# Optimization experiments

Measured on AMD Instinct MI355X. Metric: run time of the kernel, lower is better.

The kernel has to match this reference:

```python
import jax, jax.numpy as jnp
import numpy as np

E = 768          # embed_dim
H = 12           # n_attention_heads
D = E // H       # head_embed_dim = 64
S = 197          # seq_len (196 patches + CLS)
MRD = 13         # max_relative_dist
GRID = 14        # sqrt(S - 1)
B = 64
NUM_EMB = 2 * MRD + 1 + 1  # embedding table rows (index 0 reserved for CLS)


def _relative_distances(pos):
    # pos: (S-1,) int. distances clamped, shifted to [1, 2*MRD+1], padded with 0 for CLS.
    d = pos[None, :] - pos[:, None]
    d = np.clip(d, -MRD, MRD) + MRD + 1
    d = np.pad(d, ((1, 0), (1, 0)), constant_values=0)
    return jnp.asarray(d, dtype=jnp.int32)  # (S, S)


def setup_inputs() -> dict:
    key = jax.random.key(0)
    ks = jax.random.split(key, 16)
    s_lin = 1.0 / np.sqrt(E)
    inp = {
        "x": jax.random.normal(ks[0], (B, S, E), jnp.float32),
        "Wq": jax.random.normal(ks[1], (E, E), jnp.float32) * s_lin,
        "bq": jnp.zeros((E,), jnp.float32),
        "Wk": jax.random.normal(ks[2], (E, E), jnp.float32) * s_lin,
        "bk": jnp.zeros((E,), jnp.float32),
        "Wv": jax.random.normal(ks[3], (E, E), jnp.float32) * s_lin,
        "bv": jnp.zeros((E,), jnp.float32),
        "Wo": jax.random.normal(ks[4], (E, E), jnp.float32) * s_lin,
        "bo": jnp.zeros((E,), jnp.float32),
        "q_tab_x": jax.random.normal(ks[5], (NUM_EMB, D // 2), jnp.float32),
        "q_tab_y": jax.random.normal(ks[6], (NUM_EMB, D // 2), jnp.float32),
        "v_tab_x": jax.random.normal(ks[7], (NUM_EMB, D // 2), jnp.float32),
        "v_tab_y": jax.random.normal(ks[8], (NUM_EMB, D // 2), jnp.float32),
    }
    p = np.arange(S - 1)
    inp["x_dist"] = _relative_distances(p % GRID)   # (S, S) int32
    inp["y_dist"] = _relative_distances(p // GRID)  # (S, S) int32
    return inp


def reference(x, Wq, bq, Wk, bk, Wv, bv, Wo, bo,
              q_tab_x, q_tab_y, v_tab_x, v_tab_y, x_dist, y_dist):
    b, s, e = x.shape
    # QKV projections -> (b, h, s, d)
    xq = (x @ Wq.T + bq).reshape(b, s, H, D).transpose(0, 2, 1, 3)
    xk = (x @ Wk.T + bk).reshape(b, s, H, D).transpose(0, 2, 1, 3)
    xv = (x @ Wv.T + bv).reshape(b, s, H, D).transpose(0, 2, 1, 3)

    # content logits
    attn = jnp.einsum('bhqd,bhkd->bhqk', xq, xk)

    # query relative-position logits: pos embedding (q, k, d) gathered from x/y tables
    q_pos = jnp.concatenate([q_tab_x[x_dist], q_tab_y[y_dist]], axis=-1)  # (s, s, d)
    attn = attn + jnp.einsum('bhqd,qkd->bhqk', xq, q_pos)

    attn = jax.nn.softmax(attn / np.float32(np.sqrt(D)), axis=-1)

    out = jnp.einsum('bhqk,bhkd->bhqd', attn, xv)

    # value relative-position contribution
    v_pos = jnp.concatenate([v_tab_x[x_dist], v_tab_y[y_dist]], axis=-1)  # (s, s, d)
    out = out + jnp.einsum('bhqk,qkd->bhqd', attn, v_pos)

    out = out.transpose(0, 2, 1, 3).reshape(b, s, e)
    return out @ Wo.T + bo
```

## Files before the change

kernel.cpp:

```cpp
#include <hip/hip_runtime.h>
#include <math.h>

#define SEQ 197
#define EMB 768
#define NH  12
#define HD  64
#define NE  28
#define SK  208
#define VP  232
#define PP  232
#define EP  232
#define HP  68
#define TP  66
#define NW  7
#define NT  448

typedef __attribute__((ext_vector_type(8))) __bf16 bf16x8;
typedef __attribute__((ext_vector_type(4))) float  f32x4;

__device__ __forceinline__ unsigned short f2bf(float f) {
    unsigned u = __float_as_uint(f);
    u += 0x7fffu + ((u >> 16) & 1u);
    return (unsigned short)(u >> 16);
}
__device__ __forceinline__ float bfl(unsigned u) { return __uint_as_float(u << 16); }

__device__ __forceinline__ void gl_lds16(const ushort* g, ushort* l) {
    __builtin_amdgcn_global_load_lds(
        (const __attribute__((address_space(1))) unsigned int*)g,
        (__attribute__((address_space(3))) unsigned int*)l, 16, 0, 0);
}

__global__ void cvt_k(const float* __restrict__ src, ushort* __restrict__ dst, int n4) {
    int i = blockIdx.x * 256 + threadIdx.x;
    if (i < n4) {
        float4 v = ((const float4*)src)[i];
        ushort4 o = { f2bf(v.x), f2bf(v.y), f2bf(v.z), f2bf(v.w) };
        ((ushort4*)dst)[i] = o;
    }
}

__global__ void cvt_w4(const float* __restrict__ wq, const float* __restrict__ wk,
                       const float* __restrict__ wv, const float* __restrict__ wo,
                       ushort* __restrict__ wqkv, ushort* __restrict__ wob) {
    int i = blockIdx.x * 256 + threadIdx.x;
    if (i >= 4 * 147456) return;
    int seg = i / 147456, r = i - seg * 147456;
    const float* s = (seg == 0) ? wq : (seg == 1) ? wk : (seg == 2) ? wv : wo;
    float4 v = ((const float4*)s)[r];
    ushort4 o = { f2bf(v.x), f2bf(v.y), f2bf(v.z), f2bf(v.w) };
    if (seg < 3) ((ushort4*)wqkv)[(size_t)seg * 147456 + r] = o;
    else         ((ushort4*)wob)[r] = o;
}

__global__ __launch_bounds__(256) void rxy_gemm(
    const ushort* __restrict__ xq,
    const float* __restrict__ qtx, const float* __restrict__ qty,
    ushort* __restrict__ r_o)
{
    __shared__ __align__(16) ushort qtab_s[64][66];

    const int bh = blockIdx.x;
    const size_t base = (size_t)bh * SEQ * HD;
    const int tid = threadIdx.x;
    const int w = tid >> 6, lane = tid & 63;
    const int g = lane >> 4, c15 = lane & 15;

    for (int idx = tid; idx < 64 * 64; idx += 256) {
        const int e = idx >> 6, d = idx & 63;
        float v = 0.f;
        if (e < 28)      { if (d < 32)  v = qtx[e * 32 + d]; }
        else if (e < 56) { if (d >= 32) v = qty[(e - 28) * 32 + (d - 32)]; }
        qtab_s[e][d] = f2bf(v);
    }
    __syncthreads();

    for (int qt = w; qt < 13; qt += 4) {
        const int qrow = qt * 16 + c15;
        const int qld = (qrow < SEQ) ? qrow : SEQ - 1;
        const bf16x8 qa0 = *(const bf16x8*)(xq + base + (size_t)qld * HD + g * 8);
        const bf16x8 qa1 = *(const bf16x8*)(xq + base + (size_t)qld * HD + 32 + g * 8);
#pragma unroll
        for (int et = 0; et < 4; et++) {
            bf16x8 t0 = *(const bf16x8*)&qtab_s[et * 16 + c15][g * 8];
            bf16x8 t1 = *(const bf16x8*)&qtab_s[et * 16 + c15][32 + g * 8];
            f32x4 a = (f32x4)0.f;
            a = __builtin_amdgcn_mfma_f32_16x16x32_bf16(qa0, t0, a, 0, 0, 0);
            a = __builtin_amdgcn_mfma_f32_16x16x32_bf16(qa1, t1, a, 0, 0, 0);
#pragma unroll
            for (int r = 0; r < 4; r++) {
                const int q = qt * 16 + g * 4 + r;
                const int e = et * 16 + c15;
                if (q < SEQ && e < 56)
                    r_o[((size_t)bh * SEQ + q) * 56 + e] = f2bf(a[r]);
            }
        }
    }
}

template<int MODE>
__global__ __launch_bounds__(256, 2) void gemm_k64(
    const ushort* __restrict__ A, const ushort* __restrict__ W,
    const float* __restrict__ b0, const float* __restrict__ b1, const float* __restrict__ b2,
    ushort* __restrict__ q_o, ushort* __restrict__ k_o, ushort* __restrict__ v_o,
    float* __restrict__ f_o, int M)
{
    __shared__ __align__(16) ushort As[128 * 64];
    __shared__ __align__(16) ushort Bs[128 * 64];

    const int tid  = threadIdx.x;
    const int w    = tid >> 6, lane = tid & 63;
    const int wr   = w >> 1,  wc   = w & 1;

    const int nmt = gridDim.x, nnt = gridDim.y;
    const int lin = blockIdx.y * nmt + blockIdx.x;
    const int gsz = 8 * nnt;
    const int grp = lin / gsz;
    const int rr  = lin - grp * gsz;
    int mig = nmt - grp * 8; if (mig > 8) mig = 8;
    const int mt  = grp * 8 + rr % mig;
    const int nt  = rr / mig;
    const int m0  = mt * 128;
    const int n0  = nt * 128;

    int arow[4], asrc[4];
#pragma unroll
    for (int i = 0; i < 4; i++) {
        const int gidx = tid + i * 256;
        const int row = gidx >> 3, ch = gidx & 7;
        arow[i] = row;
        asrc[i] = (ch ^ (row & 7)) * 8;
    }

    f32x4 acc[4][4];
#pragma unroll
    for (int m = 0; m < 4; m++)
#pragma unroll
        for (int n = 0; n < 4; n++) acc[m][n] = (f32x4)0.f;

    for (int k0 = 0; k0 < EMB; k0 += 64) {
#pragma unroll
        for (int i = 0; i < 4; i++) {
            int ra = m0 + arow[i]; if (ra >= M) ra = M - 1;
            gl_lds16(A + (size_t)ra * EMB + k0 + asrc[i], As + (tid + i * 256) * 8);
            gl_lds16(W + (size_t)(n0 + arow[i]) * EMB + k0 + asrc[i], Bs + (tid + i * 256) * 8);
        }
        __syncthreads();

#pragma unroll
        for (int kk = 0; kk < 2; kk++) {
            bf16x8 af[4], bfr[4];
#pragma unroll
            for (int m = 0; m < 4; m++) {
                const int row = wr * 64 + m * 16 + (lane & 15);
                af[m] = *(const bf16x8*)&As[row * 64 + (((kk * 4 + (lane >> 4)) ^ (row & 7)) << 3)];
            }
#pragma unroll
            for (int n = 0; n < 4; n++) {
                const int row = wc * 64 + n * 16 + (lane & 15);
                bfr[n] = *(const bf16x8*)&Bs[row * 64 + (((kk * 4 + (lane >> 4)) ^ (row & 7)) << 3)];
            }
#pragma unroll
            for (int m = 0; m < 4; m++)
#pragma unroll
                for (int n = 0; n < 4; n++)
                    acc[m][n] = __builtin_amdgcn_mfma_f32_16x16x32_bf16(af[m], bfr[n], acc[m][n], 0, 0, 0);
        }
        __syncthreads();
    }

    const int mat = n0 / EMB;
    const int nr  = n0 - mat * EMB;
    const float* bias = (mat == 0) ? b0 : (mat == 1) ? b1 : b2;
    ushort* dst = (mat == 0) ? q_o : (mat == 1) ? k_o : v_o;

#pragma unroll
    for (int m = 0; m < 4; m++) {
#pragma unroll
        for (int r = 0; r < 4; r++) {
            const int gm = m0 + wr * 64 + m * 16 + (lane >> 4) * 4 + r;
            if (gm >= M) continue;
            const int bb = gm / SEQ, ss = gm - bb * SEQ;
#pragma unroll
            for (int n = 0; n < 4; n++) {
                const int col = nr + wc * 64 + n * 16 + (lane & 15);
                if (MODE == 0) {
                    const float v = acc[m][n][r] + bias[col];
                    dst[(((size_t)bb * NH + (col >> 6)) * SEQ + ss) * HD + (col & 63)] = f2bf(v);
                } else {
                    f_o[(size_t)gm * EMB + col] = acc[m][n][r] + b0[col];
                }
            }
        }
    }
}

__global__ __launch_bounds__(NT) void attn_mfma(
    const ushort* __restrict__ xq, const ushort* __restrict__ xk, const ushort* __restrict__ xv,
    const ushort* __restrict__ rxy_g,
    const float* __restrict__ v_tab_x, const float* __restrict__ v_tab_y,
    const int* __restrict__ x_dist, const int* __restrict__ y_dist,
    ushort* __restrict__ ao)
{
    __shared__ __align__(16) ushort K_s[SK * HD];
    __shared__ __align__(16) ushort EXYs_s[SK * 40];
    __shared__ __align__(16) ushort EXYT_s[32 * EP];
    __shared__ __align__(16) ushort VT_s[HD * VP];
    __shared__ __align__(16) ushort P_s[NW * 16 * PP];
    __shared__ __align__(16) ushort vt_s[HD * TP];
    __shared__ __align__(16) ushort h_s[NW][16][HP];

    const int bh = blockIdx.x;
    const int b  = bh / NH;
    const int h  = bh % NH;
    const size_t base = (size_t)bh * SEQ * HD;
    const ushort* __restrict__ rxy_b = rxy_g + (size_t)bh * SEQ * 56;
    const int tid = threadIdx.x;
    const int w = tid >> 6, lane = tid & 63;
    const int g = lane >> 4, c15 = lane & 15;

    for (int idx = tid; idx < SK * 8; idx += NT) {
        const int r = idx >> 3, c = idx & 7;
        uint4 v = make_uint4(0, 0, 0, 0);
        if (r < SEQ) v = *(const uint4*)(xk + base + r * HD + c * 8);
        *(uint4*)&K_s[r * HD + ((c ^ (r & 7)) << 3)] = v;
    }
    for (int idx = tid; idx < SK * 40 / 8; idx += NT)
        *(uint4*)&EXYs_s[idx * 8] = make_uint4(0, 0, 0, 0);
    for (int idx = tid; idx < 32 * EP / 8; idx += NT)
        *(uint4*)&EXYT_s[idx * 8] = make_uint4(0, 0, 0, 0);
    for (int idx = tid; idx < HD * (VP - SEQ); idx += NT) {
        const int d = idx / (VP - SEQ), k = SEQ + idx - d * (VP - SEQ);
        VT_s[d * VP + k] = 0;
    }
    for (int idx = tid; idx < NW * 16 * PP / 8; idx += NT)
        *(uint4*)&P_s[idx * 8] = make_uint4(0, 0, 0, 0);
    for (int idx = tid; idx < 16 * 8 * 13; idx += NT) {
        const int kq = idx & 15, t = idx >> 4;
        const int db = t & 7, kh = t >> 3;
        const int k = kh * 16 + kq;
        if (k >= SEQ) continue;
        uint4 v = *(const uint4*)(xv + base + k * HD + db * 8);
        ushort* col = &VT_s[(db * 8) * VP + k];
        col[0 * VP] = (ushort)(v.x); col[1 * VP] = (ushort)(v.x >> 16);
        col[2 * VP] = (ushort)(v.y); col[3 * VP] = (ushort)(v.y >> 16);
        col[4 * VP] = (ushort)(v.z); col[5 * VP] = (ushort)(v.z >> 16);
        col[6 * VP] = (ushort)(v.w); col[7 * VP] = (ushort)(v.w >> 16);
    }
    for (int idx = tid; idx < HD * 64; idx += NT) {
        const int d = idx >> 6, e = idx & 63;
        float v = 0.f;
        if (d < 32) { if (e < 28) v = v_tab_x[e * 32 + d]; }
        else        { if (e >= 28 && e < 56) v = v_tab_y[(e - 28) * 32 + (d - 32)]; }
        vt_s[d * TP + e] = f2bf(v);
    }
    __syncthreads();
    for (int k = tid; k < SEQ; k += NT) {
        const int cx = (k == 0) ? 14 : (x_dist[SEQ + k] - 14);
        const int cy = (k == 0) ? 14 : (y_dist[SEQ + k] - 14);
        const ushort one = 0x3f80;
        EXYs_s[k * 40 + cx]        = one;
        EXYs_s[k * 40 + 16 + cy]   = one;
        EXYT_s[cx * EP + k]        = one;
        EXYT_s[(16 + cy) * EP + k] = one;
    }
    __syncthreads();

    for (int qt = w; qt < 13; qt += NW) {
        const int qrow = qt * 16 + c15;
        const int qld  = (qrow < SEQ) ? qrow : (SEQ - 1);
        const bf16x8 qa0 = *(const bf16x8*)(xq + base + (size_t)qld * HD + g * 8);
        const bf16x8 qa1 = *(const bf16x8*)(xq + base + (size_t)qld * HD + 32 + g * 8);

        uint4 up;
        {
            const ushort* rrow = rxy_b + qld * 56;
            const int cxq = (qld > 0) ? (x_dist[SEQ + qld] - 14) : 0;
            const int cyq = (qld > 0) ? (y_dist[SEQ + qld] - 14) : 0;
            unsigned uu[4] = {0, 0, 0, 0};
#pragma unroll
            for (int j = 0; j < 8; j++) {
                const int c = g * 8 + j;
                ushort v;
                if (qld == 0)      v = (c == 15 || c == 31) ? (ushort)0 : rrow[(c < 16) ? 0 : 28];
                else if (c < 14)   v = rrow[c - cxq + 14];
                else if (c == 14)  v = rrow[0];
                else if (c == 15)  v = 0;
                else if (c < 30)   v = rrow[28 + (c - 16) - cyq + 14];
                else if (c == 30)  v = rrow[28];
                else               v = 0;
                uu[j >> 1] |= ((unsigned)v) << ((j & 1) * 16);
            }
            up.x = uu[0]; up.y = uu[1]; up.z = uu[2]; up.w = uu[3];
        }
        const bf16x8 qa2 = *(bf16x8*)&up;

        {
            uint4* hz = (uint4*)h_s[w];
            for (int i = lane; i < 16 * HP / 8; i += 64) hz[i] = make_uint4(0, 0, 0, 0);
        }

        const int q4 = qt * 16 + 4 * g;
        float sum[4] = {0.f, 0.f, 0.f, 0.f};

#pragma unroll
        for (int kt = 0; kt < 13; kt++) {
            const int kr = kt * 16 + c15;
            bf16x8 kf0 = *(const bf16x8*)&K_s[kr * HD + (((0 + g) ^ (kr & 7)) << 3)];
            bf16x8 kf1 = *(const bf16x8*)&K_s[kr * HD + (((4 + g) ^ (kr & 7)) << 3)];
            bf16x8 kf2 = *(const bf16x8*)&EXYs_s[kr * 40 + g * 8];
            f32x4 a = (f32x4)0.f;
            a = __builtin_amdgcn_mfma_f32_16x16x32_bf16(qa0, kf0, a, 0, 0, 0);
            a = __builtin_amdgcn_mfma_f32_16x16x32_bf16(qa1, kf1, a, 0, 0, 0);
            a = __builtin_amdgcn_mfma_f32_16x16x32_bf16(qa2, kf2, a, 0, 0, 0);
#pragma unroll
            for (int r = 0; r < 4; r++) {
                const float l = a[r] * 0.125f - 8.0f;
                const float p = (kr < SEQ) ? __expf(l) : 0.f;
                sum[r] += p;
                P_s[(w * 16 + 4 * g + r) * PP + kr] = f2bf(p);
            }
        }
        float inv[4];
#pragma unroll
        for (int r = 0; r < 4; r++) {
            sum[r] += __shfl_xor(sum[r], 1);
            sum[r] += __shfl_xor(sum[r], 2);
            sum[r] += __shfl_xor(sum[r], 4);
            sum[r] += __shfl_xor(sum[r], 8);
            inv[r] = 1.f / sum[r];
        }

        f32x4 px0 = (f32x4)0.f, px1 = (f32x4)0.f;
#pragma unroll
        for (int ks = 0; ks < 7; ks++) {
            bf16x8 pf = *(const bf16x8*)&P_s[(w * 16 + c15) * PP + ks * 32 + g * 8];
            bf16x8 e0 = *(const bf16x8*)&EXYT_s[c15 * EP + ks * 32 + g * 8];
            bf16x8 e1 = *(const bf16x8*)&EXYT_s[(16 + c15) * EP + ks * 32 + g * 8];
            px0 = __builtin_amdgcn_mfma_f32_16x16x32_bf16(pf, e0, px0, 0, 0, 0);
            px1 = __builtin_amdgcn_mfma_f32_16x16x32_bf16(pf, e1, px1, 0, 0, 0);
        }

        float sx = px0[0], sy = px1[0];
        if (qt == 0) {
            sx += __shfl_xor(sx, 1); sx += __shfl_xor(sx, 2);
            sx += __shfl_xor(sx, 4); sx += __shfl_xor(sx, 8);
            sy += __shfl_xor(sy, 1); sy += __shfl_xor(sy, 2);
            sy += __shfl_xor(sy, 4); sy += __shfl_xor(sy, 8);
        }

#pragma unroll
        for (int r = 0; r < 4; r++) {
            const int q = q4 + r;
            if (q >= SEQ) continue;
            const int ql = 4 * g + r;
            if (q == 0) {
                if (c15 == 14) { h_s[w][ql][0] = f2bf(sx); h_s[w][ql][28] = f2bf(sy); }
            } else {
                const int cxq2 = x_dist[SEQ + q] - 14;
                const int cyq2 = y_dist[SEQ + q] - 14;
                if (c15 < 14) {
                    h_s[w][ql][c15 - cxq2 + 14]      = f2bf(px0[r]);
                    h_s[w][ql][28 + c15 - cyq2 + 14] = f2bf(px1[r]);
                } else if (c15 == 14) {
                    h_s[w][ql][0]  = f2bf(px0[r]);
                    h_s[w][ql][28] = f2bf(px1[r]);
                }
            }
        }

        f32x4 o[4];
#pragma unroll
        for (int dt = 0; dt < 4; dt++) o[dt] = (f32x4)0.f;
#pragma unroll
        for (int ks = 0; ks < 7; ks++) {
            bf16x8 pf = *(const bf16x8*)&P_s[(w * 16 + c15) * PP + ks * 32 + g * 8];
#pragma unroll
            for (int dt = 0; dt < 4; dt++) {
                bf16x8 vf = *(const bf16x8*)&VT_s[(dt * 16 + c15) * VP + ks * 32 + g * 8];
                o[dt] = __builtin_amdgcn_mfma_f32_16x16x32_bf16(pf, vf, o[dt], 0, 0, 0);
            }
        }
#pragma unroll
        for (int ks2 = 0; ks2 < 2; ks2++) {
            bf16x8 hf = *(const bf16x8*)&h_s[w][c15][ks2 * 32 + g * 8];
#pragma unroll
            for (int dt = 0; dt < 4; dt++) {
                bf16x8 tf = *(const bf16x8*)&vt_s[(dt * 16 + c15) * TP + ks2 * 32 + g * 8];
                o[dt] = __builtin_amdgcn_mfma_f32_16x16x32_bf16(hf, tf, o[dt], 0, 0, 0);
            }
        }

#pragma unroll
        for (int dt = 0; dt < 4; dt++) {
            const int d = dt * 16 + c15;
#pragma unroll
            for (int r = 0; r < 4; r++) {
                const int q = q4 + r;
                if (q < SEQ)
                    ao[((size_t)(b * SEQ + q)) * EMB + h * HD + d] = f2bf(o[dt][r] * inv[r]);
            }
        }
    }
}

extern "C" void kernel_launch(void* const* d_in, const int* in_sizes, int n_in,
                              void* d_out, int out_size, void* d_ws, size_t ws_size,
                              hipStream_t stream) {
    const float* x       = (const float*)d_in[0];
    const float* Wq      = (const float*)d_in[1];
    const float* bq      = (const float*)d_in[2];
    const float* Wk      = (const float*)d_in[3];
    const float* bk      = (const float*)d_in[4];
    const float* Wv      = (const float*)d_in[5];
    const float* bv      = (const float*)d_in[6];
    const float* Wo      = (const float*)d_in[7];
    const float* bo      = (const float*)d_in[8];
    const float* q_tab_x = (const float*)d_in[9];
    const float* q_tab_y = (const float*)d_in[10];
    const float* v_tab_x = (const float*)d_in[11];
    const float* v_tab_y = (const float*)d_in[12];
    const int*   x_dist  = (const int*)d_in[13];
    const int*   y_dist  = (const int*)d_in[14];
    float* out = (float*)d_out;

    const int M  = in_sizes[0] / EMB;
    const int Bc = M / SEQ;

    ushort* xb   = (ushort*)d_ws;
    ushort* wqkv = xb   + (size_t)M * EMB;
    ushort* wob  = wqkv + (size_t)2304 * EMB;
    ushort* xqb  = wob  + (size_t)EMB * EMB;
    ushort* xkb  = xqb  + (size_t)M * EMB;
    ushort* xvb  = xkb  + (size_t)M * EMB;
    ushort* aob  = xvb  + (size_t)M * EMB;
    ushort* r_o  = aob  + (size_t)M * EMB;

    const int n4x = M * EMB / 4;
    cvt_k<<<dim3((n4x + 255) / 256), dim3(256), 0, stream>>>(x, xb, n4x);
    cvt_w4<<<dim3(2304), dim3(256), 0, stream>>>(Wq, Wk, Wv, Wo, wqkv, wob);

    gemm_k64<0><<<dim3((M + 127) / 128, 18), dim3(256), 0, stream>>>(
        xb, wqkv, bq, bk, bv, xqb, xkb, xvb, nullptr, M);

    rxy_gemm<<<dim3(Bc * NH), dim3(256), 0, stream>>>(xqb, q_tab_x, q_tab_y, r_o);

    attn_mfma<<<dim3(Bc * NH), dim3(NT), 0, stream>>>(
        xqb, xkb, xvb, r_o, v_tab_x, v_tab_y, x_dist, y_dist, aob);

    gemm_k64<1><<<dim3((M + 127) / 128, 6), dim3(256), 0, stream>>>(
        aob, wob, bo, nullptr, nullptr, nullptr, nullptr, nullptr, out, M);
}
```

Before: 161.0 us.

## Double-buffer GEMM tiles, cache distance codes in LDS, trim P_s zeroing

The projection GEMM now uses two LDS buffers and issues the next K-tile's global-to-LDS loads before computing on the current tile, so load latency can overlap MFMA work. The attention kernel packs the x/y distance codes for each key into a small LDS array and reads from it instead of repeatedly reading x_dist/y_dist from global memory. It also zeroes only the padded tail columns of P_s rather than the whole buffer, and shrinks h_s padding. Doubling the GEMM's LDS use (64KB per block) may lower occupancy under launch_bounds(256,2). Only one __syncthreads remains per iteration, so the prefetch into the other buffer may race with waves still reading it.

```diff
diff --git a/kernel.cpp b/kernel.cpp
--- a/kernel.cpp
+++ b/kernel.cpp
@@ -10,7 +10,7 @@
 #define VP  232
 #define PP  232
 #define EP  232
-#define HP  68
+#define HP  66
 #define TP  66
 #define NW  7
 #define NT  448
@@ -105,8 +105,8 @@
     ushort* __restrict__ q_o, ushort* __restrict__ k_o, ushort* __restrict__ v_o,
     float* __restrict__ f_o, int M)
 {
-    __shared__ __align__(16) ushort As[128 * 64];
-    __shared__ __align__(16) ushort Bs[128 * 64];
+    __shared__ __align__(16) ushort As[2][128 * 64];
+    __shared__ __align__(16) ushort Bs[2][128 * 64];
 
     const int tid  = threadIdx.x;
     const int w    = tid >> 6, lane = tid & 63;
@@ -138,27 +138,36 @@
 #pragma unroll
         for (int n = 0; n < 4; n++) acc[m][n] = (f32x4)0.f;
 
-    for (int k0 = 0; k0 < EMB; k0 += 64) {
+    auto STAGE = [&](int t) {
+        const int buf = t & 1, k0 = t * 64;
 #pragma unroll
         for (int i = 0; i < 4; i++) {
             int ra = m0 + arow[i]; if (ra >= M) ra = M - 1;
-            gl_lds16(A + (size_t)ra * EMB + k0 + asrc[i], As + (tid + i * 256) * 8);
-            gl_lds16(W + (size_t)(n0 + arow[i]) * EMB + k0 + asrc[i], Bs + (tid + i * 256) * 8);
-        }
-        __syncthreads();
-
+            gl_lds16(A + (size_t)ra * EMB + k0 + asrc[i], &As[buf][(tid + i * 256) * 8]);
+            gl_lds16(W + (size_t)(n0 + arow[i]) * EMB + k0 + asrc[i], &Bs[buf][(tid + i * 256) * 8]);
+        }
+    };
+
+    STAGE(0);
+    __syncthreads();
+
+    const int NKT = EMB / 64;
+    for (int t = 0; t < NKT; ++t) {
+        if (t + 1 < NKT) STAGE(t + 1);
+        const ushort* Ab = As[t & 1];
+        const ushort* Bb = Bs[t & 1];
 #pragma unroll
         for (int kk = 0; kk < 2; kk++) {
             bf16x8 af[4], bfr[4];
 #pragma unroll
             for (int m = 0; m < 4; m++) {
                 const int row = wr * 64 + m * 16 + (lane & 15);
-                af[m] = *(const bf16x8*)&As[row * 64 + (((kk * 4 + (lane >> 4)) ^ (row & 7)) << 3)];
+                af[m] = *(const bf16x8*)&Ab[row * 64 + (((kk * 4 + (lane >> 4)) ^ (row & 7)) << 3)];
             }
 #pragma unroll
             for (int n = 0; n < 4; n++) {
                 const int row = wc * 64 + n * 16 + (lane & 15);
-                bfr[n] = *(const bf16x8*)&Bs[row * 64 + (((kk * 4 + (lane >> 4)) ^ (row & 7)) << 3)];
+                bfr[n] = *(const bf16x8*)&Bb[row * 64 + (((kk * 4 + (lane >> 4)) ^ (row & 7)) << 3)];
             }
 #pragma unroll
             for (int m = 0; m < 4; m++)
@@ -209,6 +218,7 @@
     __shared__ __align__(16) ushort P_s[NW * 16 * PP];
     __shared__ __align__(16) ushort vt_s[HD * TP];
     __shared__ __align__(16) ushort h_s[NW][16][HP];
+    __shared__ ushort cxy_s[SEQ];
 
     const int bh = blockIdx.x;
     const int b  = bh / NH;
@@ -233,8 +243,12 @@
         const int d = idx / (VP - SEQ), k = SEQ + idx - d * (VP - SEQ);
         VT_s[d * VP + k] = 0;
     }
-    for (int idx = tid; idx < NW * 16 * PP / 8; idx += NT)
-        *(uint4*)&P_s[idx * 8] = make_uint4(0, 0, 0, 0);
+    for (int idx = tid; idx < NW * 16 * 3; idx += NT) {
+        const int row = idx / 3, c = idx - row * 3;
+        *(uint4*)&P_s[row * PP + 208 + c * 8] = make_uint4(0, 0, 0, 0);
+    }
+    for (int k = tid; k < SEQ; k += NT)
+        cxy_s[k] = (ushort)((x_dist[SEQ + k] & 0xff) | ((y_dist[SEQ + k] & 0xff) << 8));
     for (int idx = tid; idx < 16 * 8 * 13; idx += NT) {
         const int kq = idx & 15, t = idx >> 4;
         const int db = t & 7, kh = t >> 3;
@@ -256,8 +270,8 @@
     }
     __syncthreads();
     for (int k = tid; k < SEQ; k += NT) {
-        const int cx = (k == 0) ? 14 : (x_dist[SEQ + k] - 14);
-        const int cy = (k == 0) ? 14 : (y_dist[SEQ + k] - 14);
+        const int cx = (k == 0) ? 14 : ((cxy_s[k] & 0xff) - 14);
+        const int cy = (k == 0) ? 14 : ((cxy_s[k] >> 8) - 14);
         const ushort one = 0x3f80;
         EXYs_s[k * 40 + cx]        = one;
         EXYs_s[k * 40 + 16 + cy]   = one;
@@ -275,8 +289,8 @@
         uint4 up;
         {
             const ushort* rrow = rxy_b + qld * 56;
-            const int cxq = (qld > 0) ? (x_dist[SEQ + qld] - 14) : 0;
-            const int cyq = (qld > 0) ? (y_dist[SEQ + qld] - 14) : 0;
+            const int cxq = (qld > 0) ? ((cxy_s[qld] & 0xff) - 14) : 0;
+            const int cyq = (qld > 0) ? ((cxy_s[qld] >> 8) - 14) : 0;
             unsigned uu[4] = {0, 0, 0, 0};
 #pragma unroll
             for (int j = 0; j < 8; j++) {
@@ -357,8 +371,8 @@
             if (q == 0) {
                 if (c15 == 14) { h_s[w][ql][0] = f2bf(sx); h_s[w][ql][28] = f2bf(sy); }
             } else {
-                const int cxq2 = x_dist[SEQ + q] - 14;
-                const int cyq2 = y_dist[SEQ + q] - 14;
+                const int cxq2 = (cxy_s[q] & 0xff) - 14;
+                const int cyq2 = (cxy_s[q] >> 8) - 14;
                 if (c15 < 14) {
                     h_s[w][ql][c15 - cxq2 + 14]      = f2bf(px0[r]);
                     h_s[w][ql][28 + c15 - cyq2 + 14] = f2bf(px1[r]);
```

New measurement: 187.0 us. 1.16x slower.
